# Performance work log

Measured on AMD Instinct MI355X. Metric: run time of the kernel, lower is better.

The kernel has to match this reference:

```python
import jax, jax.numpy as jnp
import numpy as np

N_GAUSS = 512
PLANE = 512


def setup_inputs() -> dict:
    key = jax.random.key(0)
    k1, k2, k3, k4, k5 = jax.random.split(key, 5)
    mean = jax.random.uniform(k1, (N_GAUSS, 2, 1), dtype=jnp.float32)
    alpha = jax.random.uniform(k2, (N_GAUSS, 1), dtype=jnp.float32)
    scale = jax.random.uniform(k3, (N_GAUSS, 2), dtype=jnp.float32)
    theta = jax.random.uniform(k4, (N_GAUSS, 1), dtype=jnp.float32)
    rgb = jax.random.uniform(k5, (N_GAUSS, 3), dtype=jnp.float32)
    # render plane: torch.meshgrid(x, y, indexing='xy'), stack([x, y], -1)
    lin = jnp.linspace(0.0, 1.0, PLANE, dtype=jnp.float32)
    xx, yy = jnp.meshgrid(lin, lin, indexing='xy')
    pixels = jnp.stack([xx, yy], axis=-1)  # (H, W, 2)
    return {"mean": mean, "alpha": alpha, "scale": scale, "theta": theta,
            "rgb": rgb, "pixels": pixels}


def _forward(mean, alpha, scale, theta, rgb, pixels):
    two_pi = 2.0 * jnp.pi
    # covariance = R S S^T R^T with R from circular_activation(theta)
    ta = two_pi * theta                      # (N,1)
    c = jnp.cos(ta)
    s = jnp.sin(ta)
    rot = jnp.stack([jnp.concatenate([c, -s], axis=-1),
                     jnp.concatenate([s, c], axis=-1)], axis=-2)   # (N,2,2)
    smat = jnp.eye(2, dtype=scale.dtype)[None] * scale[..., None]  # (N,2,2)
    cov = rot @ smat @ jnp.swapaxes(smat, -1, -2) @ jnp.swapaxes(rot, -1, -2)
    a = cov[:, 0, 0]
    b01 = cov[:, 0, 1]
    b10 = cov[:, 1, 0]
    d = cov[:, 1, 1]
    det = a * d - b01 * b10                  # (N,)
    inv00 = d / det
    inv01 = -b01 / det
    inv10 = -b10 / det
    inv11 = a / det
    # quadratic form per pixel (analytic 2x2, same math as diff^T inv diff)
    mu = mean[:, :, 0]                       # (N,2)
    dx = pixels[None, :, :, 0] - mu[:, 0][:, None, None]  # (N,H,W)
    dy = pixels[None, :, :, 1] - mu[:, 1][:, None, None]  # (N,H,W)
    q = (inv00[:, None, None] * dx * dx
         + (inv01 + inv10)[:, None, None] * dx * dy
         + inv11[:, None, None] * dy * dy)
    prob = jnp.exp(-0.5 * q) / (two_pi * jnp.sqrt(det))[:, None, None]  # (N,H,W)
    splat = prob / jnp.max(prob)             # global max-normalize
    weighted = rgb * alpha                   # (N,3) rgb * alpha mask
    img = jnp.einsum('nhw,nc->hwc', splat, weighted)  # sum over gaussians
    return jax.nn.sigmoid(img)               # (H,W,3)


def reference(mean, alpha, scale, theta, rgb, pixels):
    return _forward(mean, alpha, scale, theta, rgb, pixels)
```

## Files before the change

kernel.cpp:

```cpp
#include <hip/hip_runtime.h>

#define NG 512
#define PLANE 512

typedef float v2f __attribute__((ext_vector_type(2)));

#define PRM_OFF  16
#define SLOT_OFF 4352

__global__ __launch_bounds__(256) void prep_kernel(
    const float* __restrict__ mean, const float* __restrict__ alpha,
    const float* __restrict__ scale, const float* __restrict__ theta,
    const float* __restrict__ rgb, float* __restrict__ ws) {
    const int n   = blockIdx.x;
    const int tid = threadIdx.x;

    const float TWO_PI = 6.283185307179586f;
    float th = theta[n];
    float c = __builtin_amdgcn_cosf(th);
    float s = __builtin_amdgcn_sinf(th);
    float sx = scale[2 * n], sy = scale[2 * n + 1];

    float m200 = (c * sx) * sx;
    float m201 = (-(s * sy)) * sy;
    float m210 = (s * sx) * sx;
    float m211 = (c * sy) * sy;
    float a   = m200 * c + m201 * (-s);
    float b01 = m200 * s + m201 * c;
    float b10 = m210 * c + m211 * (-s);
    float d   = m210 * s + m211 * c;

    float det = a * d - b01 * b10;
    float rdet = __builtin_amdgcn_rcpf(det);
    float inv00 = d * rdet;
    float inv01 = -b01 * rdet;
    float inv10 = -b10 * rdet;
    float inv11 = a * rdet;

    float norm = __builtin_amdgcn_rcpf(TWO_PI * __builtin_amdgcn_sqrtf(det));
    const float K = -0.5f * 1.4426950408889634f;

    float A_ = K * inv00;
    float B_ = K * (inv01 + inv10);
    float C_ = K * inv11;
    float mx = mean[2 * n], my = mean[2 * n + 1];
    float Lg = fmaf(-0.5f, __builtin_amdgcn_logf(det), -2.651496129472319f);

    if (tid == 0) {
        float w = alpha[n] * norm;
        float4* p = (float4*)(ws + PRM_OFF + 8 * n);
        p[0] = make_float4(A_, B_, C_, mx);
        p[1] = make_float4(my, w * rgb[3 * n], w * rgb[3 * n + 1], w * rgb[3 * n + 2]);
    }

    const float STEP = 1.0f / 511.0f;
    float inv2A = __builtin_amdgcn_rcpf(2.0f * A_);
    float t = -1e30f;
#pragma unroll
    for (int k = 0; k < 2; ++k) {
        int r = tid + (k << 8);
        float y  = (float)r * STEP;
        float dy = y - my;
        float bdy  = B_ * dy;
        float cdy2 = C_ * (dy * dy);
        float xstar = mx - bdy * inv2A;
        float xs = fminf(fmaxf(xstar, 0.0f), 1.0f);
        int i1 = min((int)(xs * 511.0f), 510);
#pragma unroll
        for (int kk = -1; kk <= 2; ++kk) {
            int i = max(0, min(i1 + kk, 511));
            float x = (float)i * STEP;
            float dx = x - mx;
            float q = fmaf(fmaf(A_, dx, bdy), dx, cdy2);
            t = fmaxf(t, q);
        }
    }
    t += Lg;

#pragma unroll
    for (int off = 32; off > 0; off >>= 1)
        t = fmaxf(t, __shfl_xor(t, off));
    __shared__ float sm[4];
    if ((tid & 63) == 0) sm[tid >> 6] = t;
    __syncthreads();
    if (tid == 0) {
        float mm = fmaxf(fmaxf(sm[0], sm[1]), fmaxf(sm[2], sm[3]));
        ws[SLOT_OFF + n] = mm;
    }
}

__global__ __launch_bounds__(512, 4) void splat_kernel(
    const float* __restrict__ pixels, const float* __restrict__ ws,
    float* __restrict__ out) {
    const int tid  = threadIdx.x;
    const int wv   = __builtin_amdgcn_readfirstlane(tid >> 6);
    const int lane = tid & 63;
    const int quad = blockIdx.x * 64 + lane;
    const int pbase = quad << 2;

    float4 p01 = *reinterpret_cast<const float4*>(pixels + 2 * pbase);
    float4 p23 = *reinterpret_cast<const float4*>(pixels + 2 * pbase + 4);
    const float y = p01.y;
    const v2f x01 = {p01.x, p01.z};
    const v2f x23 = {p23.x, p23.z};

    const float4* prm4 = reinterpret_cast<const float4*>(ws + PRM_OFF) + (wv << 7);

    v2f ar01 = {0.f, 0.f}, ag01 = {0.f, 0.f}, ab01 = {0.f, 0.f};
    v2f ar23 = {0.f, 0.f}, ag23 = {0.f, 0.f}, ab23 = {0.f, 0.f};

#pragma unroll 8
    for (int n = 0; n < 64; ++n) {
        float4 pa = prm4[2 * n];
        float4 pb = prm4[2 * n + 1];

        float a = pa.x, b = pa.y, cc = pa.z, mx = pa.w;
        float my = pb.x, wr = pb.y, wg = pb.z, wb = pb.w;

        float dy   = y - my;
        float bdy  = b * dy;
        float cdy2 = cc * (dy * dy);
        v2f bdyv  = {bdy, bdy};
        v2f cdy2v = {cdy2, cdy2};

        v2f dx01 = x01 - (v2f){mx, mx};
        v2f dx23 = x23 - (v2f){mx, mx};
        v2f t01 = __builtin_elementwise_fma(dx01, (v2f){a, a}, bdyv);
        v2f t23 = __builtin_elementwise_fma(dx23, (v2f){a, a}, bdyv);
        v2f q01 = __builtin_elementwise_fma(t01, dx01, cdy2v);
        v2f q23 = __builtin_elementwise_fma(t23, dx23, cdy2v);

        v2f e01 = {__builtin_amdgcn_exp2f(q01.x), __builtin_amdgcn_exp2f(q01.y)};
        v2f e23 = {__builtin_amdgcn_exp2f(q23.x), __builtin_amdgcn_exp2f(q23.y)};

        ar01 = __builtin_elementwise_fma(e01, (v2f){wr, wr}, ar01);
        ag01 = __builtin_elementwise_fma(e01, (v2f){wg, wg}, ag01);
        ab01 = __builtin_elementwise_fma(e01, (v2f){wb, wb}, ab01);
        ar23 = __builtin_elementwise_fma(e23, (v2f){wr, wr}, ar23);
        ag23 = __builtin_elementwise_fma(e23, (v2f){wg, wg}, ag23);
        ab23 = __builtin_elementwise_fma(e23, (v2f){wb, wb}, ab23);
    }

    __shared__ float4 red[8][64][3];
    red[wv][lane][0] = make_float4(ar01.x, ag01.x, ab01.x, ar01.y);
    red[wv][lane][1] = make_float4(ag01.y, ab01.y, ar23.x, ag23.x);
    red[wv][lane][2] = make_float4(ab23.x, ar23.y, ag23.y, ab23.y);

    float invmax = 0.f;
    if (wv == 0) {
        const float4* sl = reinterpret_cast<const float4*>(ws + SLOT_OFF) + 2 * lane;
        float4 s0 = sl[0], s1 = sl[1];
        float m = fmaxf(fmaxf(fmaxf(s0.x, s0.y), fmaxf(s0.z, s0.w)),
                        fmaxf(fmaxf(s1.x, s1.y), fmaxf(s1.z, s1.w)));
#pragma unroll
        for (int off = 32; off > 0; off >>= 1)
            m = fmaxf(m, __shfl_xor(m, off));
        invmax = __builtin_amdgcn_exp2f(-m);
    }
    __syncthreads();

    if (wv == 0) {
        float4 v0 = red[0][lane][0], v1 = red[0][lane][1], v2 = red[0][lane][2];
#pragma unroll
        for (int cch = 1; cch < 8; ++cch) {
            float4 u0 = red[cch][lane][0], u1 = red[cch][lane][1], u2 = red[cch][lane][2];
            v0.x += u0.x; v0.y += u0.y; v0.z += u0.z; v0.w += u0.w;
            v1.x += u1.x; v1.y += u1.y; v1.z += u1.z; v1.w += u1.w;
            v2.x += u2.x; v2.y += u2.y; v2.z += u2.z; v2.w += u2.w;
        }

        const float KE = 1.4426950408889634f;
#define SIG(x) __builtin_amdgcn_rcpf(1.0f + __builtin_amdgcn_exp2f(-KE * ((x) * invmax)))
        v0.x = SIG(v0.x); v0.y = SIG(v0.y); v0.z = SIG(v0.z); v0.w = SIG(v0.w);
        v1.x = SIG(v1.x); v1.y = SIG(v1.y); v1.z = SIG(v1.z); v1.w = SIG(v1.w);
        v2.x = SIG(v2.x); v2.y = SIG(v2.y); v2.z = SIG(v2.z); v2.w = SIG(v2.w);
#undef SIG

        float4* o = reinterpret_cast<float4*>(out + (size_t)pbase * 3);
        o[0] = v0; o[1] = v1; o[2] = v2;
    }
}

extern "C" void kernel_launch(void* const* d_in, const int* in_sizes, int n_in,
                              void* d_out, int out_size, void* d_ws, size_t ws_size,
                              hipStream_t stream) {
    const float* mean   = (const float*)d_in[0];
    const float* alpha  = (const float*)d_in[1];
    const float* scale  = (const float*)d_in[2];
    const float* theta  = (const float*)d_in[3];
    const float* rgb    = (const float*)d_in[4];
    const float* pixels = (const float*)d_in[5];
    float* out = (float*)d_out;
    float* ws  = (float*)d_ws;

    prep_kernel<<<512, 256, 0, stream>>>(mean, alpha, scale, theta, rgb, ws);

    splat_kernel<<<1024, 512, 0, stream>>>(pixels, ws, out);
}
```

Before: 90.16 us.

## Process eight pixels per lane, one row per block, and spread the reduction over threads

Each lane now handles 8 pixels of one image row instead of 4, so every Gaussian parameter load and the per-Gaussian dy terms are reused across twice as many pixels, and the grid is halved to one block per row. The cross-wave reduction and sigmoid epilogue are spread over 384 threads, one float4 each, instead of being done serially by wave 0, and the output is written with coalesced float4 stores. The max-slot reduction now runs in every wave. The cost is more accumulator registers, so launch bounds drop to 2 blocks per CU, which reduces occupancy for this exp-bound loop.

```diff
diff --git a/kernel.cpp b/kernel.cpp
--- a/kernel.cpp
+++ b/kernel.cpp
@@ -89,27 +89,31 @@
     }
 }
 
-__global__ __launch_bounds__(512, 4) void splat_kernel(
+__global__ __launch_bounds__(512, 2) void splat_kernel(
     const float* __restrict__ pixels, const float* __restrict__ ws,
     float* __restrict__ out) {
     const int tid  = threadIdx.x;
     const int wv   = __builtin_amdgcn_readfirstlane(tid >> 6);
     const int lane = tid & 63;
-    const int quad = blockIdx.x * 64 + lane;
-    const int pbase = quad << 2;
-
-    float4 p01 = *reinterpret_cast<const float4*>(pixels + 2 * pbase);
-    float4 p23 = *reinterpret_cast<const float4*>(pixels + 2 * pbase + 4);
-    const float y = p01.y;
-    const v2f x01 = {p01.x, p01.z};
-    const v2f x23 = {p23.x, p23.z};
+    const int row  = blockIdx.x;
+    const int px0  = (row << 9) + (lane << 3);
+
+    const float4* pp = reinterpret_cast<const float4*>(pixels + 2 * px0);
+    float4 pA = pp[0], pB = pp[1], pC = pp[2], pD = pp[3];
+    const float y = pA.y;
+    const v2f x01 = {pA.x, pA.z};
+    const v2f x23 = {pB.x, pB.z};
+    const v2f x45 = {pC.x, pC.z};
+    const v2f x67 = {pD.x, pD.z};
 
     const float4* prm4 = reinterpret_cast<const float4*>(ws + PRM_OFF) + (wv << 7);
 
     v2f ar01 = {0.f, 0.f}, ag01 = {0.f, 0.f}, ab01 = {0.f, 0.f};
     v2f ar23 = {0.f, 0.f}, ag23 = {0.f, 0.f}, ab23 = {0.f, 0.f};
-
-#pragma unroll 8
+    v2f ar45 = {0.f, 0.f}, ag45 = {0.f, 0.f}, ab45 = {0.f, 0.f};
+    v2f ar67 = {0.f, 0.f}, ag67 = {0.f, 0.f}, ab67 = {0.f, 0.f};
+
+#pragma unroll 4
     for (int n = 0; n < 64; ++n) {
         float4 pa = prm4[2 * n];
         float4 pb = prm4[2 * n + 1];
@@ -120,34 +124,43 @@
         float dy   = y - my;
         float bdy  = b * dy;
         float cdy2 = cc * (dy * dy);
+        v2f av    = {a, a};
+        v2f mxv   = {mx, mx};
         v2f bdyv  = {bdy, bdy};
         v2f cdy2v = {cdy2, cdy2};
 
-        v2f dx01 = x01 - (v2f){mx, mx};
-        v2f dx23 = x23 - (v2f){mx, mx};
-        v2f t01 = __builtin_elementwise_fma(dx01, (v2f){a, a}, bdyv);
-        v2f t23 = __builtin_elementwise_fma(dx23, (v2f){a, a}, bdyv);
+        v2f dx01 = x01 - mxv, dx23 = x23 - mxv, dx45 = x45 - mxv, dx67 = x67 - mxv;
+        v2f t01 = __builtin_elementwise_fma(dx01, av, bdyv);
+        v2f t23 = __builtin_elementwise_fma(dx23, av, bdyv);
+        v2f t45 = __builtin_elementwise_fma(dx45, av, bdyv);
+        v2f t67 = __builtin_elementwise_fma(dx67, av, bdyv);
         v2f q01 = __builtin_elementwise_fma(t01, dx01, cdy2v);
         v2f q23 = __builtin_elementwise_fma(t23, dx23, cdy2v);
+        v2f q45 = __builtin_elementwise_fma(t45, dx45, cdy2v);
+        v2f q67 = __builtin_elementwise_fma(t67, dx67, cdy2v);
 
         v2f e01 = {__builtin_amdgcn_exp2f(q01.x), __builtin_amdgcn_exp2f(q01.y)};
         v2f e23 = {__builtin_amdgcn_exp2f(q23.x), __builtin_amdgcn_exp2f(q23.y)};
-
-        ar01 = __builtin_elementwise_fma(e01, (v2f){wr, wr}, ar01);
-        ag01 = __builtin_elementwise_fma(e01, (v2f){wg, wg}, ag01);
-        ab01 = __builtin_elementwise_fma(e01, (v2f){wb, wb}, ab01);
-        ar23 = __builtin_elementwise_fma(e23, (v2f){wr, wr}, ar23);
-        ag23 = __builtin_elementwise_fma(e23, (v2f){wg, wg}, ag23);
-        ab23 = __builtin_elementwise_fma(e23, (v2f){wb, wb}, ab23);
-    }
-
-    __shared__ float4 red[8][64][3];
-    red[wv][lane][0] = make_float4(ar01.x, ag01.x, ab01.x, ar01.y);
-    red[wv][lane][1] = make_float4(ag01.y, ab01.y, ar23.x, ag23.x);
-    red[wv][lane][2] = make_float4(ab23.x, ar23.y, ag23.y, ab23.y);
-
-    float invmax = 0.f;
-    if (wv == 0) {
+        v2f e45 = {__builtin_amdgcn_exp2f(q45.x), __builtin_amdgcn_exp2f(q45.y)};
+        v2f e67 = {__builtin_amdgcn_exp2f(q67.x), __builtin_amdgcn_exp2f(q67.y)};
+
+        v2f wrv = {wr, wr}, wgv = {wg, wg}, wbv = {wb, wb};
+        ar01 = __builtin_elementwise_fma(e01, wrv, ar01);
+        ag01 = __builtin_elementwise_fma(e01, wgv, ag01);
+        ab01 = __builtin_elementwise_fma(e01, wbv, ab01);
+        ar23 = __builtin_elementwise_fma(e23, wrv, ar23);
+        ag23 = __builtin_elementwise_fma(e23, wgv, ag23);
+        ab23 = __builtin_elementwise_fma(e23, wbv, ab23);
+        ar45 = __builtin_elementwise_fma(e45, wrv, ar45);
+        ag45 = __builtin_elementwise_fma(e45, wgv, ag45);
+        ab45 = __builtin_elementwise_fma(e45, wbv, ab45);
+        ar67 = __builtin_elementwise_fma(e67, wrv, ar67);
+        ag67 = __builtin_elementwise_fma(e67, wgv, ag67);
+        ab67 = __builtin_elementwise_fma(e67, wbv, ab67);
+    }
+
+    float invmax;
+    {
         const float4* sl = reinterpret_cast<const float4*>(ws + SLOT_OFF) + 2 * lane;
         float4 s0 = sl[0], s1 = sl[1];
         float m = fmaxf(fmaxf(fmaxf(s0.x, s0.y), fmaxf(s0.z, s0.w)),
@@ -157,27 +170,30 @@
             m = fmaxf(m, __shfl_xor(m, off));
         invmax = __builtin_amdgcn_exp2f(-m);
     }
+
+    __shared__ float4 red[8][64][6];
+    red[wv][lane][0] = make_float4(ar01.x, ag01.x, ab01.x, ar01.y);
+    red[wv][lane][1] = make_float4(ag01.y, ab01.y, ar23.x, ag23.x);
+    red[wv][lane][2] = make_float4(ab23.x, ar23.y, ag23.y, ab23.y);
+    red[wv][lane][3] = make_float4(ar45.x, ag45.x, ab45.x, ar45.y);
+    red[wv][lane][4] = make_float4(ag45.y, ab45.y, ar67.x, ag67.x);
+    red[wv][lane][5] = make_float4(ab67.x, ar67.y, ag67.y, ab67.y);
     __syncthreads();
 
-    if (wv == 0) {
-        float4 v0 = red[0][lane][0], v1 = red[0][lane][1], v2 = red[0][lane][2];
+    if (tid < 384) {
+        const int l    = tid / 6;
+        const int slot = tid - 6 * l;
+        float4 v = red[0][l][slot];
 #pragma unroll
         for (int cch = 1; cch < 8; ++cch) {
-            float4 u0 = red[cch][lane][0], u1 = red[cch][lane][1], u2 = red[cch][lane][2];
-            v0.x += u0.x; v0.y += u0.y; v0.z += u0.z; v0.w += u0.w;
-            v1.x += u1.x; v1.y += u1.y; v1.z += u1.z; v1.w += u1.w;
-            v2.x += u2.x; v2.y += u2.y; v2.z += u2.z; v2.w += u2.w;
+            float4 u = red[cch][l][slot];
+            v.x += u.x; v.y += u.y; v.z += u.z; v.w += u.w;
         }
-
         const float KE = 1.4426950408889634f;
 #define SIG(x) __builtin_amdgcn_rcpf(1.0f + __builtin_amdgcn_exp2f(-KE * ((x) * invmax)))
-        v0.x = SIG(v0.x); v0.y = SIG(v0.y); v0.z = SIG(v0.z); v0.w = SIG(v0.w);
-        v1.x = SIG(v1.x); v1.y = SIG(v1.y); v1.z = SIG(v1.z); v1.w = SIG(v1.w);
-        v2.x = SIG(v2.x); v2.y = SIG(v2.y); v2.z = SIG(v2.z); v2.w = SIG(v2.w);
+        v.x = SIG(v.x); v.y = SIG(v.y); v.z = SIG(v.z); v.w = SIG(v.w);
 #undef SIG
-
-        float4* o = reinterpret_cast<float4*>(out + (size_t)pbase * 3);
-        o[0] = v0; o[1] = v1; o[2] = v2;
+        reinterpret_cast<float4*>(out)[row * 384 + tid] = v;
     }
 }
 
@@ -195,5 +211,5 @@
 
     prep_kernel<<<512, 256, 0, stream>>>(mean, alpha, scale, theta, rgb, ws);
 
-    splat_kernel<<<1024, 512, 0, stream>>>(pixels, ws, out);
+    splat_kernel<<<512, 512, 0, stream>>>(pixels, ws, out);
 }
```

Measured after the change: 91.97 us. +2.0%, slower.

## Stage per-row gaussian params in LDS and spread final reduction across threads

Applied to the files above, without the earlier changes.

Each block covers one image row, so the y-dependent terms (B*dy, C*dy^2) are computed once per gaussian per block and staged in shared memory with the other parameters. The inner loop then reads them from LDS instead of global memory and drops the per-iteration dy arithmetic. The cross-wave reduction and sigmoid are spread over 192 threads instead of one wave, and the output is written with coalesced float4 stores. The shared buffer is reused for the reduction, which adds extra barriers, and every wave now computes the global max.

```diff
diff --git a/kernel.cpp b/kernel.cpp
--- a/kernel.cpp
+++ b/kernel.cpp
@@ -97,57 +97,61 @@
     const int lane = tid & 63;
     const int quad = blockIdx.x * 64 + lane;
     const int pbase = quad << 2;
+    const int row  = blockIdx.x >> 1;
+
+    __shared__ float4 shbuf[1536];
+
+    {
+        const float4* p = reinterpret_cast<const float4*>(ws + PRM_OFF) + 2 * tid;
+        float4 p0 = p[0];
+        float4 p1 = p[1];
+        float yb = pixels[(row << 10) + 1];
+        float dy   = yb - p1.x;
+        float bdy  = p0.y * dy;
+        float cdy2 = p0.z * (dy * dy);
+        shbuf[2 * tid]     = make_float4(p0.x, p0.w, bdy, cdy2);
+        shbuf[2 * tid + 1] = make_float4(p1.y, p1.z, p1.w, 0.f);
+    }
+    __syncthreads();
 
     float4 p01 = *reinterpret_cast<const float4*>(pixels + 2 * pbase);
     float4 p23 = *reinterpret_cast<const float4*>(pixels + 2 * pbase + 4);
-    const float y = p01.y;
     const v2f x01 = {p01.x, p01.z};
     const v2f x23 = {p23.x, p23.z};
 
-    const float4* prm4 = reinterpret_cast<const float4*>(ws + PRM_OFF) + (wv << 7);
-
     v2f ar01 = {0.f, 0.f}, ag01 = {0.f, 0.f}, ab01 = {0.f, 0.f};
     v2f ar23 = {0.f, 0.f}, ag23 = {0.f, 0.f}, ab23 = {0.f, 0.f};
 
+    const float4* chunk = shbuf + (wv << 7);
 #pragma unroll 8
     for (int n = 0; n < 64; ++n) {
-        float4 pa = prm4[2 * n];
-        float4 pb = prm4[2 * n + 1];
-
-        float a = pa.x, b = pa.y, cc = pa.z, mx = pa.w;
-        float my = pb.x, wr = pb.y, wg = pb.z, wb = pb.w;
-
-        float dy   = y - my;
-        float bdy  = b * dy;
-        float cdy2 = cc * (dy * dy);
-        v2f bdyv  = {bdy, bdy};
-        v2f cdy2v = {cdy2, cdy2};
-
-        v2f dx01 = x01 - (v2f){mx, mx};
-        v2f dx23 = x23 - (v2f){mx, mx};
-        v2f t01 = __builtin_elementwise_fma(dx01, (v2f){a, a}, bdyv);
-        v2f t23 = __builtin_elementwise_fma(dx23, (v2f){a, a}, bdyv);
-        v2f q01 = __builtin_elementwise_fma(t01, dx01, cdy2v);
-        v2f q23 = __builtin_elementwise_fma(t23, dx23, cdy2v);
+        float4 ta = chunk[2 * n];
+        float4 tb = chunk[2 * n + 1];
+
+        float A_ = ta.x, mx = ta.y, bdy = ta.z, cdy2 = ta.w;
+        v2f Av = {A_, A_}, mxv = {mx, mx}, bdyv = {bdy, bdy}, cdv = {cdy2, cdy2};
+
+        v2f dx01 = x01 - mxv;
+        v2f dx23 = x23 - mxv;
+        v2f t01 = __builtin_elementwise_fma(Av, dx01, bdyv);
+        v2f t23 = __builtin_elementwise_fma(Av, dx23, bdyv);
+        v2f q01 = __builtin_elementwise_fma(t01, dx01, cdv);
+        v2f q23 = __builtin_elementwise_fma(t23, dx23, cdv);
 
         v2f e01 = {__builtin_amdgcn_exp2f(q01.x), __builtin_amdgcn_exp2f(q01.y)};
         v2f e23 = {__builtin_amdgcn_exp2f(q23.x), __builtin_amdgcn_exp2f(q23.y)};
 
-        ar01 = __builtin_elementwise_fma(e01, (v2f){wr, wr}, ar01);
-        ag01 = __builtin_elementwise_fma(e01, (v2f){wg, wg}, ag01);
-        ab01 = __builtin_elementwise_fma(e01, (v2f){wb, wb}, ab01);
-        ar23 = __builtin_elementwise_fma(e23, (v2f){wr, wr}, ar23);
-        ag23 = __builtin_elementwise_fma(e23, (v2f){wg, wg}, ag23);
-        ab23 = __builtin_elementwise_fma(e23, (v2f){wb, wb}, ab23);
-    }
-
-    __shared__ float4 red[8][64][3];
-    red[wv][lane][0] = make_float4(ar01.x, ag01.x, ab01.x, ar01.y);
-    red[wv][lane][1] = make_float4(ag01.y, ab01.y, ar23.x, ag23.x);
-    red[wv][lane][2] = make_float4(ab23.x, ar23.y, ag23.y, ab23.y);
-
-    float invmax = 0.f;
-    if (wv == 0) {
+        v2f wrv = {tb.x, tb.x}, wgv = {tb.y, tb.y}, wbv = {tb.z, tb.z};
+        ar01 = __builtin_elementwise_fma(e01, wrv, ar01);
+        ag01 = __builtin_elementwise_fma(e01, wgv, ag01);
+        ab01 = __builtin_elementwise_fma(e01, wbv, ab01);
+        ar23 = __builtin_elementwise_fma(e23, wrv, ar23);
+        ag23 = __builtin_elementwise_fma(e23, wgv, ag23);
+        ab23 = __builtin_elementwise_fma(e23, wbv, ab23);
+    }
+
+    float invmax;
+    {
         const float4* sl = reinterpret_cast<const float4*>(ws + SLOT_OFF) + 2 * lane;
         float4 s0 = sl[0], s1 = sl[1];
         float m = fmaxf(fmaxf(fmaxf(s0.x, s0.y), fmaxf(s0.z, s0.w)),
@@ -157,27 +161,31 @@
             m = fmaxf(m, __shfl_xor(m, off));
         invmax = __builtin_amdgcn_exp2f(-m);
     }
-    __syncthreads();
-
-    if (wv == 0) {
-        float4 v0 = red[0][lane][0], v1 = red[0][lane][1], v2 = red[0][lane][2];
+
+    __syncthreads();
+
+    {
+        const int base = ((wv << 6) + lane) * 3;
+        shbuf[base + 0] = make_float4(ar01.x, ag01.x, ab01.x, ar01.y);
+        shbuf[base + 1] = make_float4(ag01.y, ab01.y, ar23.x, ag23.x);
+        shbuf[base + 2] = make_float4(ab23.x, ar23.y, ag23.y, ab23.y);
+    }
+    __syncthreads();
+
+    if (tid < 192) {
+        const int l    = tid / 3;
+        const int slot = tid - 3 * l;
+        float4 v = shbuf[l * 3 + slot];
 #pragma unroll
         for (int cch = 1; cch < 8; ++cch) {
-            float4 u0 = red[cch][lane][0], u1 = red[cch][lane][1], u2 = red[cch][lane][2];
-            v0.x += u0.x; v0.y += u0.y; v0.z += u0.z; v0.w += u0.w;
-            v1.x += u1.x; v1.y += u1.y; v1.z += u1.z; v1.w += u1.w;
-            v2.x += u2.x; v2.y += u2.y; v2.z += u2.z; v2.w += u2.w;
+            float4 u = shbuf[((cch << 6) + l) * 3 + slot];
+            v.x += u.x; v.y += u.y; v.z += u.z; v.w += u.w;
         }
-
         const float KE = 1.4426950408889634f;
 #define SIG(x) __builtin_amdgcn_rcpf(1.0f + __builtin_amdgcn_exp2f(-KE * ((x) * invmax)))
-        v0.x = SIG(v0.x); v0.y = SIG(v0.y); v0.z = SIG(v0.z); v0.w = SIG(v0.w);
-        v1.x = SIG(v1.x); v1.y = SIG(v1.y); v1.z = SIG(v1.z); v1.w = SIG(v1.w);
-        v2.x = SIG(v2.x); v2.y = SIG(v2.y); v2.z = SIG(v2.z); v2.w = SIG(v2.w);
+        v.x = SIG(v.x); v.y = SIG(v.y); v.z = SIG(v.z); v.w = SIG(v.w);
 #undef SIG
-
-        float4* o = reinterpret_cast<float4*>(out + (size_t)pbase * 3);
-        o[0] = v0; o[1] = v1; o[2] = v2;
+        reinterpret_cast<float4*>(out)[blockIdx.x * 192 + tid] = v;
     }
 }
 
```

New measurement: 91.04 us. About the same (+1.0%).
